# Performance work log

Measured on AMD Instinct MI355X. Metric: run time of the kernel, lower is better.

## Reference

```python
import jax, jax.numpy as jnp
import numpy as np
from jax import lax

B, C, H, W, P = 16, 256, 64, 64, 4
EPS = 1e-5


def setup_inputs() -> dict:
    key = jax.random.key(0)
    ks = jax.random.split(key, 16)
    s = 0.05
    d = {
        'rgb': jax.random.normal(ks[0], (B, C, H, W), jnp.float32),
        'th': jax.random.normal(ks[1], (B, C, H, W), jnp.float32),
        'q_w': jax.random.normal(ks[2], (C, C), jnp.float32) * s,
        'q_b': jax.random.normal(ks[3], (C,), jnp.float32) * s,
        'kvr_w': jax.random.normal(ks[4], (2 * C, C), jnp.float32) * s,
        'kvr_b': jax.random.normal(ks[5], (2 * C,), jnp.float32) * s,
        'kvt_w': jax.random.normal(ks[6], (2 * C, C), jnp.float32) * s,
        'kvt_b': jax.random.normal(ks[7], (2 * C,), jnp.float32) * s,
        'offr_w': jax.random.normal(ks[8], (2 * P, C, 3, 3), jnp.float32) * s,
        'offr_b': jax.random.normal(ks[9], (2 * P,), jnp.float32) * s,
        'offt_w': jax.random.normal(ks[10], (2 * P, C, 3, 3), jnp.float32) * s,
        'offt_b': jax.random.normal(ks[11], (2 * P,), jnp.float32) * s,
        'out_w': jax.random.normal(ks[12], (C, 2 * C), jnp.float32) * s,
        'out_b': jax.random.normal(ks[13], (C,), jnp.float32) * s,
        'gamma': jnp.ones((C,), jnp.float32),
        'beta': jnp.zeros((C,), jnp.float32),
    }
    return d


def conv1x1(x, w, b):
    # x: [B,Ci,H,W], w: [Co,Ci] -> [B,Co,H,W]
    return jnp.einsum('bchw,oc->bohw', x, w) + b[None, :, None, None]


def conv3x3(x, w, b):
    y = lax.conv_general_dilated(x, w, (1, 1), 'SAME',
                                 dimension_numbers=('NCHW', 'OIHW', 'NCHW'))
    return y + b[None, :, None, None]


def deform_sample(feat, offset):
    # feat: [B,C,H,W]; offset: [B,2P,H,W] (pixel-unit offsets, (x,y) pairs)
    Bs, Cs, Hs, Ws = feat.shape
    off = offset.reshape(Bs, -1, 2, Hs, Ws)  # [B,P,2,H,W]
    # base grid in [-1,1], align_corners=True convention
    gy = jnp.linspace(-1.0, 1.0, Hs)[None, None, :, None]
    gx = jnp.linspace(-1.0, 1.0, Ws)[None, None, None, :]
    grid_x = gx + off[:, :, 0] / (Ws / 2.0)  # [B,P,H,W]
    grid_y = gy + off[:, :, 1] / (Hs / 2.0)
    # normalized -> pixel coords (align_corners=True)
    x = (grid_x + 1.0) * (Ws - 1) / 2.0
    y = (grid_y + 1.0) * (Hs - 1) / 2.0
    x0 = jnp.floor(x)
    y0 = jnp.floor(y)
    wx = x - x0
    wy = y - y0
    feat_flat = feat.reshape(Bs, Cs, Hs * Ws)

    def corner(xi, yi, wgt):
        valid = (xi >= 0) & (xi < Ws) & (yi >= 0) & (yi < Hs)  # zeros padding
        xc = jnp.clip(xi, 0, Ws - 1).astype(jnp.int32)
        yc = jnp.clip(yi, 0, Hs - 1).astype(jnp.int32)
        idx = (yc * Ws + xc).reshape(Bs, 1, -1)  # [B,1,P*H*W]
        g = jnp.take_along_axis(feat_flat, jnp.broadcast_to(idx, (Bs, Cs, idx.shape[-1])), axis=2)
        g = g.reshape(Bs, Cs, -1, Hs, Ws)  # [B,C,P,H,W]
        w_eff = (wgt * valid.astype(feat.dtype))[:, None]  # [B,1,P,H,W]
        return g * w_eff

    x0i = x0.astype(jnp.int32)
    y0i = y0.astype(jnp.int32)
    out = (corner(x0i, y0i, (1 - wx) * (1 - wy))
           + corner(x0i + 1, y0i, wx * (1 - wy))
           + corner(x0i, y0i + 1, (1 - wx) * wy)
           + corner(x0i + 1, y0i + 1, wx * wy))
    return out.mean(axis=2)  # mean over P -> [B,C,H,W]


def batchnorm_train(x, gamma, beta):
    mu = x.mean(axis=(0, 2, 3), keepdims=True)
    var = x.var(axis=(0, 2, 3), keepdims=True)
    xn = (x - mu) * lax.rsqrt(var + EPS)
    return xn * gamma[None, :, None, None] + beta[None, :, None, None]


def reference(rgb, th, q_w, q_b, kvr_w, kvr_b, kvt_w, kvt_b,
              offr_w, offr_b, offt_w, offt_b, out_w, out_b, gamma, beta):
    q_rgb = conv1x1(rgb, q_w, q_b)
    q_th = conv1x1(th, q_w, q_b)
    kv_rgb = conv1x1(rgb, kvr_w, kvr_b)
    kv_th = conv1x1(th, kvt_w, kvt_b)
    v_rgb = kv_rgb[:, C:]  # k_rgb = kv_rgb[:, :C] is unused downstream
    v_th = kv_th[:, C:]
    off_rgb2th = conv3x3(th, offr_w, offr_b)
    off_th2rgb = conv3x3(rgb, offt_w, offt_b)
    v_rgb2th = deform_sample(v_rgb, off_rgb2th)
    v_th2rgb = deform_sample(v_th, off_th2rgb)
    attn_rgb = jax.nn.sigmoid(q_rgb) * v_th2rgb
    attn_th = jax.nn.sigmoid(q_th) * v_rgb2th
    fused = conv1x1(jnp.concatenate([attn_rgb, attn_th], axis=1), out_w, out_b)
    return batchnorm_train(fused + 0.5 * (rgb + th), gamma, beta)
```

## Files before the change

kernel.cpp:

```cpp
#include <hip/hip_runtime.h>

typedef __bf16 bf16x8 __attribute__((ext_vector_type(8)));
typedef float  f32x4  __attribute__((ext_vector_type(4)));
typedef float  f32x2  __attribute__((ext_vector_type(2)));

constexpr int Bn = 16, Cn = 256, Hn = 64, Wn = 64, HWn = 64 * 64;
constexpr int Ntot = Bn * HWn;

#define DEV static __device__ __forceinline__

DEV unsigned short f2bf(float f) {
  unsigned u = __builtin_bit_cast(unsigned, f);
  u += 0x7fffu + ((u >> 16) & 1u);
  return (unsigned short)(u >> 16);
}
DEV float bf2f(unsigned short s) {
  unsigned u = ((unsigned)s) << 16;
  return __builtin_bit_cast(float, u);
}
DEV bf16x8 asbf(uint4 u) { return __builtin_bit_cast(bf16x8, u); }

__global__ void k_prep(const float* qw, const float* kvrw, const float* kvtw,
                       const float* offrw, const float* offtw, const float* outw,
                       unsigned short* Aqv, unsigned short* Aoff, unsigned short* Aout) {
  int idx = blockIdx.x * 256 + threadIdx.x;
  if (idx < 2 * 512 * 256) {
    int t = idx >> 17; int r = idx & 131071; int o = r >> 8; int c = r & 255;
    float v = (o < 256) ? qw[o * 256 + c] : (t ? kvtw[o * 256 + c] : kvrw[o * 256 + c]);
    Aqv[idx] = f2bf(v);
    return;
  }
  idx -= 2 * 512 * 256;
  if (idx < 2 * 16 * 2304) {
    int t = idx / 36864; int r = idx % 36864;
    int o = r / 2304; int rc = r % 2304; int tap = rc >> 8; int c = rc & 255;
    const float* w = t ? offtw : offrw;
    float v = (o < 8) ? w[(o * 256 + c) * 9 + tap] : 0.f;
    Aoff[idx] = f2bf(v);
    return;
  }
  idx -= 2 * 16 * 2304;
  if (idx < 256 * 512) {
    int seg = idx >> 11, o = (idx >> 3) & 255, e = idx & 7;
    Aout[idx] = f2bf(outw[o * 512 + seg * 8 + e]);
  }
}

__global__ void k_transpose(const float* rgb, const float* th, unsigned short* xT) {
  int bi = blockIdx.x;
  int ct = bi & 3;
  int nt = (bi >> 2) & 63;
  int b  = (bi >> 8) & 15;
  int t  = bi >> 12;
  const float* src = t ? th : rgb;
  int c0 = ct * 64, n0 = nt * 64;
  __shared__ float tile[64][65];
  int tid = threadIdx.x;
  int nl = tid & 63, cg = tid >> 6;
#pragma unroll
  for (int i = 0; i < 16; i++) {
    int c = cg * 16 + i;
    tile[c][nl] = src[(size_t)(b * 256 + c0 + c) * HWn + n0 + nl];
  }
  __syncthreads();
  int pr = tid >> 2, sg = tid & 3;
  unsigned short tmp[16];
#pragma unroll
  for (int j = 0; j < 16; j++) tmp[j] = f2bf(tile[sg * 16 + j][pr]);
  unsigned short* dst = xT + (size_t)t * Ntot * 256 +
                        (size_t)(b * HWn + n0 + pr) * 256 + c0 + sg * 16;
  *(uint4*)(dst)     = *(const uint4*)(tmp);
  *(uint4*)(dst + 8) = *(const uint4*)(tmp + 8);
}

__global__ __launch_bounds__(512, 2) void k_qv(
    const unsigned short* Aqv, const unsigned short* xT,
    const float* qb, const float* kvrb, const float* kvtb,
    unsigned short* qs, unsigned short* vv) {
  __shared__ unsigned short smem[32768];
  int t  = blockIdx.z;
  int mt = blockIdx.y;
  int nt = blockIdx.x;
  int swznt = ((nt & 7) << 6) | (nt >> 3);
  int o0 = mt * 128;
  int n0 = swznt * 128;
  int tid = threadIdx.x;
  const unsigned short* Aq = Aqv + t * 512 * 256;
  const unsigned short* Xg = xT + (size_t)t * Ntot * 256 + (size_t)n0 * 256;

  auto stage = [&](int kb, int bb) {
    unsigned short* As = smem + bb * 8192;
    unsigned short* Xs = smem + 16384 + bb * 8192;
#pragma unroll
    for (int i = 0; i < 2; i++) {
      int cid = tid + i * 512;
      int row = cid >> 3, seg = cid & 7;
      int ss = seg ^ (row & 7);
      *(uint4*)(&As[row * 64 + seg * 8]) =
          *(const uint4*)(Aq + (size_t)(o0 + row) * 256 + kb * 64 + ss * 8);
    }
#pragma unroll
    for (int i = 0; i < 2; i++) {
      int cid = tid + i * 512;
      int row = cid >> 3, seg = cid & 7;
      int ss = seg ^ (row & 7);
      *(uint4*)(&Xs[row * 64 + seg * 8]) =
          *(const uint4*)(Xg + (size_t)row * 256 + kb * 64 + ss * 8);
    }
  };

  int w = __builtin_amdgcn_readfirstlane(tid >> 6);
  int lane = tid & 63;
  int wo = w & 1, wn = w >> 1;
  int r16 = lane & 15, q4 = lane >> 4;

  f32x4 acc[4][2];
#pragma unroll
  for (int a = 0; a < 4; a++) { acc[a][0] = f32x4{0.f,0.f,0.f,0.f}; acc[a][1] = f32x4{0.f,0.f,0.f,0.f}; }

  stage(0, 0);
  __syncthreads();
#pragma unroll
  for (int kb = 0; kb < 4; kb++) {
    if (kb < 3) stage(kb + 1, (kb + 1) & 1);
    const unsigned short* As = smem + (kb & 1) * 8192;
    const unsigned short* Xs = smem + 16384 + (kb & 1) * 8192;
#pragma unroll
    for (int ks = 0; ks < 2; ks++) {
      uint4 af[4], bfr[2];
#pragma unroll
      for (int oi = 0; oi < 4; oi++) {
        int row = wo * 64 + oi * 16 + r16;
        int seg = (ks * 4 + q4) ^ (row & 7);
        af[oi] = *(const uint4*)(&As[row * 64 + seg * 8]);
      }
#pragma unroll
      for (int ni = 0; ni < 2; ni++) {
        int row = wn * 32 + ni * 16 + r16;
        int seg = (ks * 4 + q4) ^ (row & 7);
        bfr[ni] = *(const uint4*)(&Xs[row * 64 + seg * 8]);
      }
#pragma unroll
      for (int oi = 0; oi < 4; oi++)
#pragma unroll
        for (int ni = 0; ni < 2; ni++)
          acc[oi][ni] = __builtin_amdgcn_mfma_f32_16x16x32_bf16(
              asbf(af[oi]), asbf(bfr[ni]), acc[oi][ni], 0, 0, 0);
    }
    __syncthreads();
  }

  bool isq = (mt < 2);
  const float* bias = isq ? qb : (t ? kvtb : kvrb);
  float4 bv[4];
#pragma unroll
  for (int oi = 0; oi < 4; oi++)
    bv[oi] = *(const float4*)(&bias[o0 + wo * 64 + oi * 16 + q4 * 4]);
#pragma unroll
  for (int oi = 0; oi < 4; oi++) {
    int ol = wo * 64 + oi * 16 + q4 * 4;
#pragma unroll
    for (int ni = 0; ni < 2; ni++) {
      int nl = wn * 32 + ni * 16 + r16;
      unsigned short pk[4];
#pragma unroll
      for (int j = 0; j < 4; j++) {
        float val = acc[oi][ni][j] + ((const float*)&bv[oi])[j];
        if (isq) val = 1.f / (1.f + __expf(-val));
        pk[j] = f2bf(val);
      }
      *(uint2*)(&smem[nl * 132 + ol]) = *(const uint2*)(pk);
    }
  }
  __syncthreads();
  unsigned short* outp = (isq ? qs : vv) + (size_t)t * Ntot * 256 + (mt & 1) * 128;
#pragma unroll
  for (int pass = 0; pass < 4; pass++) {
    int nl = pass * 32 + (tid >> 4);
    int c  = tid & 15;
    uint4 vq = *(const uint4*)(&smem[nl * 132 + c * 8]);
    *(uint4*)(outp + (size_t)(n0 + nl) * 256 + c * 8) = vq;
  }
}

__global__ __launch_bounds__(256, 4) void k_off(
    const unsigned short* Aoff, const unsigned short* xT,
    const float* offrb, const float* offtb, float* offo) {
  __shared__ unsigned short Alds[9 * 8 * 264 + 264];
  int t  = blockIdx.y;
  int bh = blockIdx.x;
  int swz = ((bh & 7) << 7) | (bh >> 3);
  int b = swz >> 6, h = swz & 63;
  int tid = threadIdx.x;
  const unsigned short* Aw = Aoff + t * 36864;

#pragma unroll
  for (int i = 0; i < 9; i++) {
    int cid = tid + i * 256;
    int o = cid / 288;
    int rem = cid - o * 288;
    int tap = rem >> 5, cg = rem & 31;
    uint4 v = *(const uint4*)(Aw + o * 2304 + tap * 256 + cg * 8);
    *(uint4*)(&Alds[(tap * 8 + o) * 264 + cg * 8]) = v;
  }
  if (tid < 33) {
    uint4 z; z.x = 0; z.y = 0; z.z = 0; z.w = 0;
    *(uint4*)(&Alds[19008 + tid * 8]) = z;
  }
  __syncthreads();

  int lane = tid & 63, w = tid >> 6;
  int r16 = lane & 15, q4 = lane >> 4;
  int wl = w * 16 + r16;
  const unsigned short* xin = xT + (size_t)(t ? 0 : 1) * Ntot * 256;
  int zbase = 19008 + q4 * 8;
  int abase = r16 * 264 + q4 * 8;
  bool rowok = (r16 < 8);

  f32x4 acc = {0.f, 0.f, 0.f, 0.f};
  uint4 bufA[8], bufB[8];

#define LOADT(buf, tap) {                                                      \
    int dy = (tap) / 3 - 1, dx = (tap) % 3 - 1;                                \
    int hh = h + dy, ww = wl + dx;                                             \
    bool ok = (hh >= 0 && hh < 64 && ww >= 0 && ww < 64);                      \
    int hc = hh < 0 ? 0 : (hh > 63 ? 63 : hh);                                 \
    int wc = ww < 0 ? 0 : (ww > 63 ? 63 : ww);                                 \
    const unsigned short* p =                                                  \
        xin + (size_t)(((b * 64 + hc) * 64 + wc) * 256) + q4 * 8;              \
    _Pragma("unroll") for (int ks = 0; ks < 8; ks++) {                         \
      uint4 v = *(const uint4*)(p + ks * 32);                                  \
      if (!ok) { v.x = 0; v.y = 0; v.z = 0; v.w = 0; }                         \
      buf[ks] = v;                                                             \
    } }

#define COMPT(buf, tap) {                                                      \
    _Pragma("unroll") for (int ks = 0; ks < 8; ks++) {                         \
      int aofs = rowok ? ((tap) * 8 * 264 + abase + ks * 32) : (zbase + ks * 32); \
      uint4 af = *(const uint4*)(&Alds[aofs]);                                 \
      acc = __builtin_amdgcn_mfma_f32_16x16x32_bf16(asbf(af), asbf(buf[ks]),   \
                                                    acc, 0, 0, 0);             \
    } }

  LOADT(bufA, 0)
  LOADT(bufB, 1)
  COMPT(bufA, 0)
  LOADT(bufA, 2)
  COMPT(bufB, 1)
  LOADT(bufB, 3)
  COMPT(bufA, 2)
  LOADT(bufA, 4)
  COMPT(bufB, 3)
  LOADT(bufB, 5)
  COMPT(bufA, 4)
  LOADT(bufA, 6)
  COMPT(bufB, 5)
  LOADT(bufB, 7)
  COMPT(bufA, 6)
  LOADT(bufA, 8)
  COMPT(bufB, 7)
  COMPT(bufA, 8)
#undef LOADT
#undef COMPT

  if (lane < 32) {
    const float* ob = t ? offtb : offrb;
    int n = (b * 64 + h) * 64 + wl;
    float4 r;
    r.x = acc[0] + ob[q4 * 4 + 0];
    r.y = acc[1] + ob[q4 * 4 + 1];
    r.z = acc[2] + ob[q4 * 4 + 2];
    r.w = acc[3] + ob[q4 * 4 + 3];
    *(float4*)(offo + (size_t)t * Ntot * 8 + (size_t)n * 8 + q4 * 4) = r;
  }
}

DEV void addrw(int px, int h, int b, int c0, float dx, float dy,
               int* coff, float* cwgt) {
  float xf = (float)px + dx * (63.f / 64.f);
  float yf = (float)h  + dy * (63.f / 64.f);
  float x0f = floorf(xf), y0f = floorf(yf);
  float wx = xf - x0f, wy = yf - y0f;
  int x0 = (int)x0f, y0 = (int)y0f;
#pragma unroll
  for (int c = 0; c < 4; c++) {
    int cy2 = c >> 1, cx2 = c & 1;
    int ix = x0 + cx2, iy = y0 + cy2;
    bool ok = (ix >= 0 && ix < 64 && iy >= 0 && iy < 64);
    int ixc = ix < 0 ? 0 : (ix > 63 ? 63 : ix);
    int iyc = iy < 0 ? 0 : (iy > 63 ? 63 : iy);
    float wgt = (cx2 ? wx : 1.f - wx) * (cy2 ? wy : 1.f - wy);
    cwgt[c] = ok ? wgt : 0.f;
    coff[c] = ((b * 64 + iyc) * 64 + ixc) * 256 + c0;
  }
}

__global__ __launch_bounds__(512, 4) void k_fuse(
    const unsigned short* qs, const unsigned short* vv, const float* offo,
    const unsigned short* Apk, const float* outb,
    const float* rgb, const float* th, float* dout) {
  __shared__ unsigned short cc[16 * 512];
  int tid = threadIdx.x;
  int bi  = blockIdx.x;
  int swz = ((bi & 7) << 9) | (bi >> 3);
  int b = swz >> 8;
  int h = (swz >> 2) & 63;
  int px0 = (swz & 3) * 16;

  {
    int pxL = tid >> 5, chunk = tid & 31;
    int px = px0 + pxL;
    int n = (b * 64 + h) * 64 + px;
    int c0 = chunk * 8;
    int sw = pxL & 7;
#pragma unroll
    for (int pass = 0; pass < 2; pass++) {
      const unsigned short* vsrc = vv + (size_t)(pass ? 0 : 1) * Ntot * 256;
      const float* offp = offo + (size_t)(pass ? 0 : 1) * Ntot * 8 + (size_t)n * 8;
      const unsigned short* qsrc = qs + (size_t)(pass ? 1 : 0) * Ntot * 256 + (size_t)n * 256;
      uint4  q0  = *(const uint4*)(qsrc + c0);
      float4 of0 = *(const float4*)(offp);
      float4 of1 = *(const float4*)(offp + 4);
      f32x2 accv[4];
#pragma unroll
      for (int i = 0; i < 4; i++) accv[i] = f32x2{0.f, 0.f};

      int   coffA[4], coffB[4];
      float cwgtA[4], cwgtB[4];
      uint4 bufA[4], bufB[4];
#define LOADG(buf, co) { _Pragma("unroll") for (int c2 = 0; c2 < 4; c2++)      \
        buf[c2] = *(const uint4*)(vsrc + co[c2]); }
#define FMAG(buf, cw) { _Pragma("unroll") for (int c2 = 0; c2 < 4; c2++) {     \
        f32x2 w2 = {cw[c2], cw[c2]};                                           \
        const unsigned* uu = (const unsigned*)&buf[c2];                        \
        _Pragma("unroll") for (int j2 = 0; j2 < 4; j2++) {                     \
          f32x2 v2 = { __builtin_bit_cast(float, uu[j2] << 16),                \
                       __builtin_bit_cast(float, uu[j2] & 0xffff0000u) };      \
          accv[j2] = __builtin_elementwise_fma(v2, w2, accv[j2]); } } }
      addrw(px, h, b, c0, of0.x, of0.y, coffA, cwgtA);
      LOADG(bufA, coffA)
      addrw(px, h, b, c0, of0.z, of0.w, coffB, cwgtB);
      LOADG(bufB, coffB)
      FMAG(bufA, cwgtA)
      addrw(px, h, b, c0, of1.x, of1.y, coffA, cwgtA);
      LOADG(bufA, coffA)
      FMAG(bufB, cwgtB)
      addrw(px, h, b, c0, of1.z, of1.w, coffB, cwgtB);
      LOADG(bufB, coffB)
      FMAG(bufA, cwgtA)
      FMAG(bufB, cwgtB)
#undef LOADG
#undef FMAG
      const unsigned* qu = (const unsigned*)&q0;
      unsigned pk2[4];
#pragma unroll
      for (int j2 = 0; j2 < 4; j2++) {
        f32x2 q2 = { __builtin_bit_cast(float, qu[j2] << 16),
                     __builtin_bit_cast(float, qu[j2] & 0xffff0000u) };
        f32x2 r2 = accv[j2] * q2 * 0.25f;
        unsigned ow;
        asm("v_cvt_pk_bf16_f32 %0, %1, %2" : "=v"(ow) : "v"(r2.x), "v"(r2.y));
        pk2[j2] = ow;
      }
      uint4 pkv;
      pkv.x = pk2[0]; pkv.y = pk2[1]; pkv.z = pk2[2]; pkv.w = pk2[3];
      *(uint4*)(&cc[pxL * 512 + ((pass * 32 + chunk) ^ sw) * 8]) = pkv;
    }
  }
  __syncthreads();

  int lane = tid & 63, wv = tid >> 6;
  int r16 = lane & 15, q4 = lane >> 4;
  f32x4 acc2[2];
  acc2[0] = f32x4{0.f, 0.f, 0.f, 0.f};
  acc2[1] = f32x4{0.f, 0.f, 0.f, 0.f};
#pragma unroll
  for (int kst = 0; kst < 16; kst++) {
    int slot = (kst * 4 + q4) ^ (r16 & 7);
    uint4 bfr = *(const uint4*)(&cc[r16 * 512 + slot * 8]);
#pragma unroll
    for (int oi = 0; oi < 2; oi++) {
      int o = wv * 32 + oi * 16 + r16;
      uint4 a = *(const uint4*)(Apk + (size_t)((kst * 4 + q4) * 256 + o) * 8);
      acc2[oi] = __builtin_amdgcn_mfma_f32_16x16x32_bf16(asbf(a), asbf(bfr), acc2[oi], 0, 0, 0);
    }
  }
#pragma unroll
  for (int oi = 0; oi < 2; oi++) {
    int ob = wv * 32 + oi * 16 + q4 * 4;
#pragma unroll
    for (int j = 0; j < 4; j++) {
      int o = ob + j;
      int hw = h * 64 + px0 + r16;
      size_t gidx = (size_t)(b * 256 + o) * HWn + hw;
      dout[gidx] = acc2[oi][j] + outb[o] + 0.5f * (rgb[gidx] + th[gidx]);
    }
  }
}

__global__ void k_stats(const float* dout, const float* gamma, const float* beta,
                        float* sstats) {
  int c = blockIdx.x, tid = threadIdx.x;
  float s1 = 0.f, s2 = 0.f;
#pragma unroll
  for (int b2 = 0; b2 < 16; b2++) {
    const float4* p = (const float4*)(dout + (size_t)(b2 * 256 + c) * HWn);
    for (int i = tid; i < 1024; i += 256) {
      float4 v = p[i];
      s1 += v.x + v.y + v.z + v.w;
      s2 += v.x * v.x + v.y * v.y + v.z * v.z + v.w * v.w;
    }
  }
  __shared__ float r1[256], r2[256];
  r1[tid] = s1; r2[tid] = s2;
  __syncthreads();
  for (int st = 128; st > 0; st >>= 1) {
    if (tid < st) { r1[tid] += r1[tid + st]; r2[tid] += r2[tid + st]; }
    __syncthreads();
  }
  if (tid == 0) {
    float mean = r1[0] / 65536.f;
    float var  = r2[0] / 65536.f - mean * mean;
    float scale = gamma[c] / sqrtf(var + 1e-5f);
    sstats[c]       = scale;
    sstats[256 + c] = beta[c] - mean * scale;
  }
}

__global__ void k_bn(float* dout, const float* sstats) {
  int idx = blockIdx.x * 256 + threadIdx.x;
  size_t base = (size_t)idx * 4;
  int c = (int)((base >> 12) & 255);
  float4 v = *(float4*)(dout + base);
  float sc = sstats[c], sh = sstats[256 + c];
  v.x = v.x * sc + sh; v.y = v.y * sc + sh;
  v.z = v.z * sc + sh; v.w = v.w * sc + sh;
  *(float4*)(dout + base) = v;
}

extern "C" void kernel_launch(void* const* d_in, const int* in_sizes, int n_in,
                              void* d_out, int out_size, void* d_ws, size_t ws_size,
                              hipStream_t stream) {
  const float* rgb   = (const float*)d_in[0];
  const float* th    = (const float*)d_in[1];
  const float* qw    = (const float*)d_in[2];
  const float* qb    = (const float*)d_in[3];
  const float* kvrw  = (const float*)d_in[4];
  const float* kvrb  = (const float*)d_in[5];
  const float* kvtw  = (const float*)d_in[6];
  const float* kvtb  = (const float*)d_in[7];
  const float* offrw = (const float*)d_in[8];
  const float* offrb = (const float*)d_in[9];
  const float* offtw = (const float*)d_in[10];
  const float* offtb = (const float*)d_in[11];
  const float* outw  = (const float*)d_in[12];
  const float* outb  = (const float*)d_in[13];
  const float* gamma = (const float*)d_in[14];
  const float* beta  = (const float*)d_in[15];
  float* dout = (float*)d_out;

  unsigned short* xT   = (unsigned short*)d_ws;
  unsigned short* qsb  = xT  + (size_t)2 * Ntot * 256;
  unsigned short* vvb  = qsb + (size_t)2 * Ntot * 256;
  float* offo          = (float*)(vvb + (size_t)2 * Ntot * 256);
  unsigned short* Aqv  = (unsigned short*)(offo + (size_t)2 * Ntot * 8);
  unsigned short* Aoff = Aqv + 2 * 512 * 256;
  unsigned short* Aout = Aoff + 2 * 16 * 2304;
  float* sstats        = (float*)(Aout + 256 * 512);

  k_prep<<<1824, 256, 0, stream>>>(qw, kvrw, kvtw, offrw, offtw, outw, Aqv, Aoff, Aout);
  k_transpose<<<8192, 256, 0, stream>>>(rgb, th, xT);
  k_qv<<<dim3(512, 4, 2), 512, 0, stream>>>(Aqv, xT, qb, kvrb, kvtb, qsb, vvb);
  k_off<<<dim3(1024, 2), 256, 0, stream>>>(Aoff, xT, offrb, offtb, offo);
  k_fuse<<<4096, 512, 0, stream>>>(qsb, vvb, offo, Aout, outb, rgb, th, dout);
  k_stats<<<256, 256, 0, stream>>>(dout, gamma, beta, sstats);
  k_bn<<<16384, 256, 0, stream>>>(dout, sstats);
}
```

Before: 405.4 us.

## Remap qv grid for XCD locality and split deform gather passes across threads

The qv GEMM grid is flattened so that the four M-tiles sharing an N-tile land on the same XCD, with consecutive N-tiles grouped per XCD, to improve L2 reuse of the activation tile. In the fuse kernel, each thread now handles one pass (rgb or th direction) with 16 channels instead of both passes with 8 channels each. This halves the serial dependency chain per thread but doubles the gather width per load. The LDS row stride is padded from 512 to 520 to reduce bank conflicts, at the cost of more registers per thread in the gather.

Measured after the change: 417.6 us. 1.03x slower.

```diff
diff --git a/kernel.cpp b/kernel.cpp
--- a/kernel.cpp
+++ b/kernel.cpp
@@ -78,12 +78,13 @@
     const float* qb, const float* kvrb, const float* kvtb,
     unsigned short* qs, unsigned short* vv) {
   __shared__ unsigned short smem[32768];
-  int t  = blockIdx.z;
-  int mt = blockIdx.y;
-  int nt = blockIdx.x;
-  int swznt = ((nt & 7) << 6) | (nt >> 3);
+  int t  = blockIdx.y;
+  int bi = blockIdx.x;
+  int xcd = bi & 7, loc = bi >> 3;
+  int mt = loc & 3;
+  int nt = xcd * 64 + (loc >> 2);
   int o0 = mt * 128;
-  int n0 = swznt * 128;
+  int n0 = nt * 128;
   int tid = threadIdx.x;
   const unsigned short* Aq = Aqv + t * 512 * 256;
   const unsigned short* Xg = xT + (size_t)t * Ntot * 256 + (size_t)n0 * 256;
@@ -299,7 +300,7 @@
     const unsigned short* qs, const unsigned short* vv, const float* offo,
     const unsigned short* Apk, const float* outb,
     const float* rgb, const float* th, float* dout) {
-  __shared__ unsigned short cc[16 * 512];
+  __shared__ unsigned short cc[16 * 520];
   int tid = threadIdx.x;
   int bi  = blockIdx.x;
   int swz = ((bi & 7) << 9) | (bi >> 3);
@@ -308,64 +309,78 @@
   int px0 = (swz & 3) * 16;
 
   {
-    int pxL = tid >> 5, chunk = tid & 31;
+    int pxL = tid >> 5;
+    int pass = (tid >> 4) & 1;
+    int chunk = tid & 15;
     int px = px0 + pxL;
     int n = (b * 64 + h) * 64 + px;
-    int c0 = chunk * 8;
+    int c0 = chunk * 16;
     int sw = pxL & 7;
-#pragma unroll
-    for (int pass = 0; pass < 2; pass++) {
-      const unsigned short* vsrc = vv + (size_t)(pass ? 0 : 1) * Ntot * 256;
-      const float* offp = offo + (size_t)(pass ? 0 : 1) * Ntot * 8 + (size_t)n * 8;
-      const unsigned short* qsrc = qs + (size_t)(pass ? 1 : 0) * Ntot * 256 + (size_t)n * 256;
-      uint4  q0  = *(const uint4*)(qsrc + c0);
-      float4 of0 = *(const float4*)(offp);
-      float4 of1 = *(const float4*)(offp + 4);
-      f32x2 accv[4];
-#pragma unroll
-      for (int i = 0; i < 4; i++) accv[i] = f32x2{0.f, 0.f};
-
-      int   coffA[4], coffB[4];
-      float cwgtA[4], cwgtB[4];
-      uint4 bufA[4], bufB[4];
-#define LOADG(buf, co) { _Pragma("unroll") for (int c2 = 0; c2 < 4; c2++)      \
-        buf[c2] = *(const uint4*)(vsrc + co[c2]); }
-#define FMAG(buf, cw) { _Pragma("unroll") for (int c2 = 0; c2 < 4; c2++) {     \
-        f32x2 w2 = {cw[c2], cw[c2]};                                           \
-        const unsigned* uu = (const unsigned*)&buf[c2];                        \
-        _Pragma("unroll") for (int j2 = 0; j2 < 4; j2++) {                     \
-          f32x2 v2 = { __builtin_bit_cast(float, uu[j2] << 16),                \
-                       __builtin_bit_cast(float, uu[j2] & 0xffff0000u) };      \
-          accv[j2] = __builtin_elementwise_fma(v2, w2, accv[j2]); } } }
-      addrw(px, h, b, c0, of0.x, of0.y, coffA, cwgtA);
-      LOADG(bufA, coffA)
-      addrw(px, h, b, c0, of0.z, of0.w, coffB, cwgtB);
-      LOADG(bufB, coffB)
-      FMAG(bufA, cwgtA)
-      addrw(px, h, b, c0, of1.x, of1.y, coffA, cwgtA);
-      LOADG(bufA, coffA)
-      FMAG(bufB, cwgtB)
-      addrw(px, h, b, c0, of1.z, of1.w, coffB, cwgtB);
-      LOADG(bufB, coffB)
-      FMAG(bufA, cwgtA)
-      FMAG(bufB, cwgtB)
-#undef LOADG
-#undef FMAG
-      const unsigned* qu = (const unsigned*)&q0;
-      unsigned pk2[4];
-#pragma unroll
-      for (int j2 = 0; j2 < 4; j2++) {
-        f32x2 q2 = { __builtin_bit_cast(float, qu[j2] << 16),
-                     __builtin_bit_cast(float, qu[j2] & 0xffff0000u) };
-        f32x2 r2 = accv[j2] * q2 * 0.25f;
-        unsigned ow;
-        asm("v_cvt_pk_bf16_f32 %0, %1, %2" : "=v"(ow) : "v"(r2.x), "v"(r2.y));
-        pk2[j2] = ow;
-      }
-      uint4 pkv;
-      pkv.x = pk2[0]; pkv.y = pk2[1]; pkv.z = pk2[2]; pkv.w = pk2[3];
-      *(uint4*)(&cc[pxL * 512 + ((pass * 32 + chunk) ^ sw) * 8]) = pkv;
-    }
+    const unsigned short* vsrc = vv + (size_t)(pass ? 0 : 1) * Ntot * 256;
+    const float* offp = offo + (size_t)(pass ? 0 : 1) * Ntot * 8 + (size_t)n * 8;
+    const unsigned short* qsrc = qs + (size_t)(pass ? 1 : 0) * Ntot * 256 + (size_t)n * 256;
+    uint4  q0  = *(const uint4*)(qsrc + c0);
+    uint4  q1  = *(const uint4*)(qsrc + c0 + 8);
+    float4 of0 = *(const float4*)(offp);
+    float4 of1 = *(const float4*)(offp + 4);
+    f32x2 accv[8];
+#pragma unroll
+    for (int i = 0; i < 8; i++) accv[i] = f32x2{0.f, 0.f};
+
+    int coff[4]; float cwgt[4];
+#define FMA2(LO, HI, W) { f32x2 w2 = {(W), (W)};                               \
+    const unsigned* ua = (const unsigned*)&(LO);                               \
+    const unsigned* ub = (const unsigned*)&(HI);                               \
+    _Pragma("unroll") for (int j2 = 0; j2 < 4; j2++) {                         \
+      f32x2 v2 = { __builtin_bit_cast(float, ua[j2] << 16),                    \
+                   __builtin_bit_cast(float, ua[j2] & 0xffff0000u) };          \
+      accv[j2] = __builtin_elementwise_fma(v2, w2, accv[j2]);                  \
+      f32x2 v3 = { __builtin_bit_cast(float, ub[j2] << 16),                    \
+                   __builtin_bit_cast(float, ub[j2] & 0xffff0000u) };          \
+      accv[4 + j2] = __builtin_elementwise_fma(v3, w2, accv[4 + j2]); } }
+#define GATHER_PT(DX, DY) {                                                    \
+    addrw(px, h, b, c0, (DX), (DY), coff, cwgt);                               \
+    uint4 b0 = *(const uint4*)(vsrc + coff[0]);                                \
+    uint4 b1 = *(const uint4*)(vsrc + coff[0] + 8);                            \
+    uint4 b2 = *(const uint4*)(vsrc + coff[1]);                                \
+    uint4 b3 = *(const uint4*)(vsrc + coff[1] + 8);                            \
+    FMA2(b0, b1, cwgt[0])                                                      \
+    FMA2(b2, b3, cwgt[1])                                                      \
+    b0 = *(const uint4*)(vsrc + coff[2]);                                      \
+    b1 = *(const uint4*)(vsrc + coff[2] + 8);                                  \
+    b2 = *(const uint4*)(vsrc + coff[3]);                                      \
+    b3 = *(const uint4*)(vsrc + coff[3] + 8);                                  \
+    FMA2(b0, b1, cwgt[2])                                                      \
+    FMA2(b2, b3, cwgt[3]) }
+    GATHER_PT(of0.x, of0.y)
+    GATHER_PT(of0.z, of0.w)
+    GATHER_PT(of1.x, of1.y)
+    GATHER_PT(of1.z, of1.w)
+#undef GATHER_PT
+#undef FMA2
+    unsigned pk2[8];
+    const unsigned* qu0 = (const unsigned*)&q0;
+    const unsigned* qu1 = (const unsigned*)&q1;
+#pragma unroll
+    for (int j2 = 0; j2 < 4; j2++) {
+      f32x2 qa = { __builtin_bit_cast(float, qu0[j2] << 16),
+                   __builtin_bit_cast(float, qu0[j2] & 0xffff0000u) };
+      f32x2 ra = accv[j2] * qa * 0.25f;
+      unsigned ow;
+      asm("v_cvt_pk_bf16_f32 %0, %1, %2" : "=v"(ow) : "v"(ra.x), "v"(ra.y));
+      pk2[j2] = ow;
+      f32x2 qb2 = { __builtin_bit_cast(float, qu1[j2] << 16),
+                    __builtin_bit_cast(float, qu1[j2] & 0xffff0000u) };
+      f32x2 rb = accv[4 + j2] * qb2 * 0.25f;
+      asm("v_cvt_pk_bf16_f32 %0, %1, %2" : "=v"(ow) : "v"(rb.x), "v"(rb.y));
+      pk2[4 + j2] = ow;
+    }
+    uint4 pkv0; pkv0.x = pk2[0]; pkv0.y = pk2[1]; pkv0.z = pk2[2]; pkv0.w = pk2[3];
+    uint4 pkv1; pkv1.x = pk2[4]; pkv1.y = pk2[5]; pkv1.z = pk2[6]; pkv1.w = pk2[7];
+    int slot0 = (pass * 32 + chunk * 2)     ^ sw;
+    int slot1 = (pass * 32 + chunk * 2 + 1) ^ sw;
+    *(uint4*)(&cc[pxL * 520 + slot0 * 8]) = pkv0;
+    *(uint4*)(&cc[pxL * 520 + slot1 * 8]) = pkv1;
   }
   __syncthreads();
 
@@ -377,7 +392,7 @@
 #pragma unroll
   for (int kst = 0; kst < 16; kst++) {
     int slot = (kst * 4 + q4) ^ (r16 & 7);
-    uint4 bfr = *(const uint4*)(&cc[r16 * 512 + slot * 8]);
+    uint4 bfr = *(const uint4*)(&cc[r16 * 520 + slot * 8]);
 #pragma unroll
     for (int oi = 0; oi < 2; oi++) {
       int o = wv * 32 + oi * 16 + r16;
@@ -470,7 +485,7 @@
 
   k_prep<<<1824, 256, 0, stream>>>(qw, kvrw, kvtw, offrw, offtw, outw, Aqv, Aoff, Aout);
   k_transpose<<<8192, 256, 0, stream>>>(rgb, th, xT);
-  k_qv<<<dim3(512, 4, 2), 512, 0, stream>>>(Aqv, xT, qb, kvrb, kvtb, qsb, vvb);
+  k_qv<<<dim3(2048, 2), 512, 0, stream>>>(Aqv, xT, qb, kvrb, kvtb, qsb, vvb);
   k_off<<<dim3(1024, 2), 256, 0, stream>>>(Aoff, xT, offrb, offtb, offo);
   k_fuse<<<4096, 512, 0, stream>>>(qsb, vvb, offo, Aout, outb, rgb, th, dout);
   k_stats<<<256, 256, 0, stream>>>(dout, gamma, beta, sstats);
```
